# Performance work log

Hardware: AMD Instinct MI355X
Metric: run time of the kernel (lower is better)

## Reference

```python
import jax, jax.numpy as jnp
import numpy as np

DIM = 2048
N_HEADS = 16
HEAD_DIM = 128
EPS = 1e-6


def setup_inputs() -> dict:
    key = jax.random.key(0)
    ks = jax.random.split(key, 8)
    b, gf, gh, gw = 1, 8, 16, 24
    s = gf * gh * gw
    c = HEAD_DIM // 2
    w = lambda k: 0.02 * jax.random.normal(k, (DIM, DIM), jnp.float32)
    return {
        "x": jax.random.normal(ks[0], (b, s, DIM), jnp.float32),
        "freqs_angle": jax.random.normal(ks[1], (1024, c), jnp.float32),
        "Wq": w(ks[2]), "bq": jnp.zeros((DIM,), jnp.float32),
        "Wk": w(ks[3]), "bk": jnp.zeros((DIM,), jnp.float32),
        "Wv": w(ks[4]), "bv": jnp.zeros((DIM,), jnp.float32),
        "Wo": w(ks[5]), "bo": jnp.zeros((DIM,), jnp.float32),
        "gq": jnp.ones((DIM,), jnp.float32),
        "gk": jnp.ones((DIM,), jnp.float32),
        "seq_len": s, "grid_f": gf, "grid_h": gh, "grid_w": gw,
    }


def _rms(t, g):
    return t * jax.lax.rsqrt(jnp.mean(t * t, axis=-1, keepdims=True) + EPS) * g


def _grid_angles(freqs_angle, gf, gh, gw, c):
    # band split [c - 2*(c//3), c//3, c//3] as in rope_apply
    cf = c - 2 * (c // 3)
    ch = cw = c // 3
    af = freqs_angle[:gf, :cf]            # [F, cf]
    ah = freqs_angle[:gh, cf:cf + ch]     # [H, ch]
    aw = freqs_angle[:gw, cf + ch:c]      # [W, cw]
    ang = jnp.concatenate([
        jnp.broadcast_to(af[:, None, None, :], (gf, gh, gw, cf)),
        jnp.broadcast_to(ah[None, :, None, :], (gf, gh, gw, ch)),
        jnp.broadcast_to(aw[None, None, :, :], (gf, gh, gw, cw)),
    ], axis=-1)
    return ang.reshape(gf * gh * gw, c)   # [s, c]


def reference(x, freqs_angle, Wq, bq, Wk, bk, Wv, bv, Wo, bo, gq, gk,
              seq_len, grid_f, grid_h, grid_w):
    b, s, _ = x.shape
    n, d = N_HEADS, HEAD_DIM
    c = d // 2
    ang = _grid_angles(freqs_angle, grid_f, grid_h, grid_w, c)
    cos = jnp.cos(ang)[None, :, None, :]  # [1, s, 1, c]
    sin = jnp.sin(ang)[None, :, None, :]

    def rope(t):  # complex multiply on (even, odd) = (real, imag) pairs
        te, to = t[..., 0::2], t[..., 1::2]
        return jnp.stack([te * cos - to * sin, te * sin + to * cos], axis=-1).reshape(t.shape)

    q = _rms(x @ Wq.T + bq, gq).reshape(b, s, n, d)
    k = _rms(x @ Wk.T + bk, gk).reshape(b, s, n, d)
    v = (x @ Wv.T + bv).reshape(b, s, n, d)
    q, k = rope(q), rope(k)

    scale = np.float32(1.0 / np.sqrt(d))
    scores = jnp.einsum('bqnd,bknd->bnqk', q, k) * scale
    p = jax.nn.softmax(scores, axis=-1)
    o = jnp.einsum('bnqk,bknd->bqnd', p, v).reshape(b, s, n * d)
    return o @ Wo.T + bo
```

## Files before the change

kernel.cpp:

```cpp
#include <hip/hip_runtime.h>
#include <stdint.h>
#include <stddef.h>

typedef __bf16 bf16_t;
typedef __bf16 bf16x8 __attribute__((ext_vector_type(8)));
typedef __bf16 bf16x4 __attribute__((ext_vector_type(4)));
typedef __bf16 bf16x2 __attribute__((ext_vector_type(2)));
typedef float  f32x4  __attribute__((ext_vector_type(4)));

#define SEQ   3072
#define DIMD  2048
#define NH    16
#define HD    128
#define QKVN  6144

__device__ __forceinline__ void async16(const bf16_t* g, bf16_t* l) {
  __builtin_amdgcn_global_load_lds((const __attribute__((address_space(1))) uint32_t*)g,
                                   (__attribute__((address_space(3))) uint32_t*)l, 16, 0, 0);
}

__global__ __launch_bounds__(256) void cvt_all(const float* __restrict__ x,
                                               const float* __restrict__ Wq,
                                               const float* __restrict__ Wk,
                                               const float* __restrict__ Wv,
                                               const float* __restrict__ Wo,
                                               const float* __restrict__ bq,
                                               const float* __restrict__ bk,
                                               const float* __restrict__ bv,
                                               bf16_t* __restrict__ xb,
                                               bf16_t* __restrict__ Wqkvb,
                                               bf16_t* __restrict__ Wob,
                                               float* __restrict__ bqkv) {
  const int b = blockIdx.x;
  const float* src; bf16_t* dst; int off;
  if (b < 3072)       { src = x;  dst = xb;              off = b; }
  else if (b < 5120)  { src = Wq; dst = Wqkvb;           off = b - 3072; }
  else if (b < 7168)  { src = Wk; dst = Wqkvb + 4194304; off = b - 5120; }
  else if (b < 9216)  { src = Wv; dst = Wqkvb + 8388608; off = b - 7168; }
  else if (b < 11264) { src = Wo; dst = Wob;             off = b - 9216; }
  else {
    int t = (b - 11264) * 256 + threadIdx.x;
    float v;
    if (t < 2048)      v = bq[t];
    else if (t < 4096) v = bk[t - 2048];
    else               v = bv[t - 4096];
    bqkv[t] = v;
    return;
  }
  const int idx = (off * 256 + threadIdx.x) * 8;
  const float4 a = *(const float4*)(src + idx);
  const float4 c = *(const float4*)(src + idx + 4);
  bf16x8 o;
  o[0] = (bf16_t)a.x; o[1] = (bf16_t)a.y; o[2] = (bf16_t)a.z; o[3] = (bf16_t)a.w;
  o[4] = (bf16_t)c.x; o[5] = (bf16_t)c.y; o[6] = (bf16_t)c.z; o[7] = (bf16_t)c.w;
  *(bf16x8*)(dst + idx) = o;
}

template<bool OUT_BF16>
__global__ __launch_bounds__(256, 2) void gemm_nt(const bf16_t* __restrict__ A,
                                                  const bf16_t* __restrict__ B,
                                                  const float* __restrict__ bias,
                                                  void* __restrict__ Cout,
                                                  int M, int N, int K) {
  __shared__ __align__(16) bf16_t As[128 * 64];
  __shared__ __align__(16) bf16_t Bs[128 * 64];
  const int t = threadIdx.x;
  const int lane = t & 63, wave = t >> 6;
  const int quad = lane >> 4, l15 = lane & 15;
  const int wy = wave >> 1, wx = wave & 1;
  const size_t bm = (size_t)blockIdx.y * 128, bn = (size_t)blockIdx.x * 128;
  const bf16_t* Ab = A + bm * K;
  const bf16_t* Bb = B + bn * K;
  f32x4 acc[4][4] = {};
  int srow[4], scol[4];
#pragma unroll
  for (int r = 0; r < 4; r++) {
    int L = r * 256 + t;
    int row = L >> 3, cp = L & 7;
    srow[r] = row;
    scol[r] = (cp ^ (row & 7)) * 8;
  }
  for (int k0 = 0; k0 < K; k0 += 64) {
    __syncthreads();
#pragma unroll
    for (int r = 0; r < 4; r++)
      async16(Ab + (size_t)srow[r] * K + k0 + scol[r], &As[(r * 256 + t) * 8]);
#pragma unroll
    for (int r = 0; r < 4; r++)
      async16(Bb + (size_t)srow[r] * K + k0 + scol[r], &Bs[(r * 256 + t) * 8]);
    __syncthreads();
#pragma unroll
    for (int ks = 0; ks < 2; ks++) {
      bf16x8 af[4], bfv[4];
#pragma unroll
      for (int i = 0; i < 4; i++) {
        int row = wy * 64 + i * 16 + l15;
        af[i] = *(const bf16x8*)&As[row * 64 + (((ks * 4 + quad) ^ (row & 7)) * 8)];
      }
#pragma unroll
      for (int j = 0; j < 4; j++) {
        int row = wx * 64 + j * 16 + l15;
        bfv[j] = *(const bf16x8*)&Bs[row * 64 + (((ks * 4 + quad) ^ (row & 7)) * 8)];
      }
#pragma unroll
      for (int i = 0; i < 4; i++)
#pragma unroll
        for (int j = 0; j < 4; j++)
          acc[i][j] = __builtin_amdgcn_mfma_f32_16x16x32_bf16(af[i], bfv[j], acc[i][j], 0, 0, 0);
    }
  }
#pragma unroll
  for (int i = 0; i < 4; i++) {
#pragma unroll
    for (int j = 0; j < 4; j++) {
      size_t row = bm + wy * 64 + i * 16 + quad * 4;
      size_t col = bn + wx * 64 + j * 16 + l15;
      float bb = bias[col];
#pragma unroll
      for (int r = 0; r < 4; r++) {
        float v = acc[i][j][r] + bb;
        if (OUT_BF16) ((bf16_t*)Cout)[(row + r) * N + col] = (bf16_t)v;
        else          ((float*)Cout)[(row + r) * N + col] = v;
      }
    }
  }
}

__global__ __launch_bounds__(256) void rmsrope(bf16_t* __restrict__ qkv,
                                               bf16_t* __restrict__ pk,
                                               const float* __restrict__ gq,
                                               const float* __restrict__ gk,
                                               const float* __restrict__ freqs) {
  const int s = blockIdx.x, t = threadIdx.x;
  bf16_t* row = qkv + (size_t)s * QKVN;
  bf16x8 qv = *(const bf16x8*)&row[t * 8];
  bf16x8 kv = *(const bf16x8*)&row[2048 + t * 8];
  float qf[8], kf[8];
  float qs = 0.f, ks2 = 0.f;
#pragma unroll
  for (int i = 0; i < 8; i++) {
    qf[i] = (float)qv[i]; qs  += qf[i] * qf[i];
    kf[i] = (float)kv[i]; ks2 += kf[i] * kf[i];
  }
#pragma unroll
  for (int m = 1; m < 64; m <<= 1) {
    qs  += __shfl_xor(qs, m);
    ks2 += __shfl_xor(ks2, m);
  }
  __shared__ float red[2][4];
  const int wave = t >> 6, lane = t & 63;
  if (lane == 0) { red[0][wave] = qs; red[1][wave] = ks2; }
  __syncthreads();
  qs  = red[0][0] + red[0][1] + red[0][2] + red[0][3];
  ks2 = red[1][0] + red[1][1] + red[1][2] + red[1][3];
  const float qsc = rsqrtf(qs  / 2048.f + 1e-6f);
  const float ksc = rsqrtf(ks2 / 2048.f + 1e-6f);
  const int sf = s / 384, rem = s - sf * 384;
  const int sh = rem / 24, sw = rem - sh * 24;
  bf16x8 qo, ko;
#pragma unroll
  for (int u = 0; u < 4; u++) {
    const int col = t * 8 + 2 * u;
    const int i = (col >> 1) & 63;
    const int frow = (i < 22) ? sf : ((i < 43) ? sh : sw);
    const float ang = freqs[frow * 64 + i];
    float sn, cs;
    __sincosf(ang, &sn, &cs);
    float te = qf[2 * u]     * qsc * gq[col];
    float to = qf[2 * u + 1] * qsc * gq[col + 1];
    qo[2 * u]     = (bf16_t)(te * cs - to * sn);
    qo[2 * u + 1] = (bf16_t)(te * sn + to * cs);
    te = kf[2 * u]     * ksc * gk[col];
    to = kf[2 * u + 1] * ksc * gk[col + 1];
    ko[2 * u]     = (bf16_t)(te * cs - to * sn);
    ko[2 * u + 1] = (bf16_t)(te * sn + to * cs);
  }
  *(bf16x8*)&row[t * 8] = qo;
  *(bf16x8*)&pk[((size_t)(t >> 4) * SEQ + s) * HD + (t & 15) * 8] = ko;
}

__global__ __launch_bounds__(256) void vtrans(const bf16_t* __restrict__ qkv,
                                              bf16_t* __restrict__ pvt) {
  __shared__ bf16_t tile[128][65];
  const int h = blockIdx.y;
  const int s0 = blockIdx.x * 64;
  const int t = threadIdx.x;
#pragma unroll
  for (int r = 0; r < 4; r++) {
    int L = r * 256 + t, s = L >> 4, cp = L & 15;
    bf16x8 v = *(const bf16x8*)&qkv[(size_t)(s0 + s) * QKVN + 4096 + h * HD + cp * 8];
#pragma unroll
    for (int i = 0; i < 8; i++) tile[cp * 8 + i][s] = v[i];
  }
  __syncthreads();
#pragma unroll
  for (int r = 0; r < 4; r++) {
    int L = r * 256 + t, d = L >> 3, c = L & 7;
    bf16x8 o;
#pragma unroll
    for (int i = 0; i < 8; i++) o[i] = tile[d][c * 8 + i];
    *(bf16x8*)&pvt[((size_t)h * HD + d) * SEQ + s0 + c * 8] = o;
  }
}

__global__ __launch_bounds__(256, 2) void flash_attn(const bf16_t* __restrict__ qkv,
                                                     const bf16_t* __restrict__ pk,
                                                     const bf16_t* __restrict__ pvt,
                                                     bf16_t* __restrict__ ob) {
  __shared__ __align__(16) bf16_t Ks[2][64 * 128];
  __shared__ __align__(16) bf16_t Vt[2][128 * 64];
  __shared__ __align__(16) bf16_t Ps[4][32 * 64];
  const int h = blockIdx.y, qt = blockIdx.x;
  const int s0 = qt * 128;
  const int t = threadIdx.x, wave = t >> 6, lane = t & 63;
  const int quad = lane >> 4, l15 = lane & 15;
  const int wq = wave * 32;
  const float scale = 0.08838834764831845f;
  const bf16_t* pkh = pk  + (size_t)h * (SEQ * HD);
  const bf16_t* pvh = pvt + (size_t)h * (HD * SEQ);
  int krow4[4], kc4[4], vd4[4], vc4[4];
#pragma unroll
  for (int r = 0; r < 4; r++) {
    int L = r * 256 + t;
    krow4[r] = L >> 4; kc4[r] = (L & 15) ^ (krow4[r] & 7);
    vd4[r]   = L >> 3; vc4[r] = (L & 7)  ^ (vd4[r] & 7);
  }
  bf16x8 qfr[2][4];
#pragma unroll
  for (int tj = 0; tj < 2; tj++)
#pragma unroll
    for (int ks = 0; ks < 4; ks++)
      qfr[tj][ks] = *(const bf16x8*)&qkv[(size_t)(s0 + wq + tj * 16 + l15) * QKVN + h * HD + ks * 32 + quad * 8];
  f32x4 oacc[2][8] = {};
  float m_run[2] = {-3e38f, -3e38f}, l_run[2] = {0.f, 0.f};
#pragma unroll
  for (int r = 0; r < 4; r++) {
    int L = r * 256 + t;
    async16(pkh + (size_t)krow4[r] * HD + kc4[r] * 8, &Ks[0][L * 8]);
  }
#pragma unroll
  for (int r = 0; r < 4; r++) {
    int L = r * 256 + t;
    async16(pvh + (size_t)vd4[r] * SEQ + vc4[r] * 8, &Vt[0][L * 8]);
  }
  for (int kt = 0; kt < SEQ / 64; kt++) {
    const int cur = kt & 1;
    __syncthreads();
    if (kt + 1 < SEQ / 64) {
      const int kv1 = (kt + 1) * 64;
#pragma unroll
      for (int r = 0; r < 4; r++) {
        int L = r * 256 + t;
        async16(pkh + (size_t)(kv1 + krow4[r]) * HD + kc4[r] * 8, &Ks[cur ^ 1][L * 8]);
      }
#pragma unroll
      for (int r = 0; r < 4; r++) {
        int L = r * 256 + t;
        async16(pvh + (size_t)vd4[r] * SEQ + kv1 + vc4[r] * 8, &Vt[cur ^ 1][L * 8]);
      }
    }
    f32x4 st[4][2] = {};
#pragma unroll
    for (int ks = 0; ks < 4; ks++) {
      bf16x8 kfr[4];
#pragma unroll
      for (int ti = 0; ti < 4; ti++) {
        const int kr = ti * 16 + l15;
        kfr[ti] = *(const bf16x8*)&Ks[cur][kr * 128 + (((ks * 4 + quad) ^ (kr & 7)) * 8)];
      }
#pragma unroll
      for (int ti = 0; ti < 4; ti++)
#pragma unroll
        for (int tj = 0; tj < 2; tj++)
          st[ti][tj] = __builtin_amdgcn_mfma_f32_16x16x32_bf16(kfr[ti], qfr[tj][ks], st[ti][tj], 0, 0, 0);
    }
    float mt[2] = {-3e38f, -3e38f};
#pragma unroll
    for (int ti = 0; ti < 4; ti++)
#pragma unroll
      for (int tj = 0; tj < 2; tj++)
#pragma unroll
        for (int r = 0; r < 4; r++) {
          st[ti][tj][r] *= scale;
          mt[tj] = fmaxf(mt[tj], st[ti][tj][r]);
        }
    float al[2];
#pragma unroll
    for (int tj = 0; tj < 2; tj++) {
      mt[tj] = fmaxf(mt[tj], __shfl_xor(mt[tj], 16));
      mt[tj] = fmaxf(mt[tj], __shfl_xor(mt[tj], 32));
      const float mn = fmaxf(m_run[tj], mt[tj]);
      al[tj] = __expf(m_run[tj] - mn);
      m_run[tj] = mn;
    }
    float lt[2] = {0.f, 0.f};
#pragma unroll
    for (int ti = 0; ti < 4; ti++)
#pragma unroll
      for (int tj = 0; tj < 2; tj++) {
        bf16x4 pv;
#pragma unroll
        for (int r = 0; r < 4; r++) {
          const float p = __expf(st[ti][tj][r] - m_run[tj]);
          pv[r] = (bf16_t)p;
          lt[tj] += (float)pv[r];
        }
        const int q = tj * 16 + l15;
        const int cp2 = (ti * 2 + (quad >> 1)) ^ (q & 7);
        *(bf16x4*)&Ps[wave][q * 64 + cp2 * 8 + (quad & 1) * 4] = pv;
      }
#pragma unroll
    for (int tj = 0; tj < 2; tj++) {
      lt[tj] += __shfl_xor(lt[tj], 16);
      lt[tj] += __shfl_xor(lt[tj], 32);
      l_run[tj] = l_run[tj] * al[tj] + lt[tj];
    }
#pragma unroll
    for (int ti = 0; ti < 2; ti++) {
      float a0 = __shfl(al[ti], quad * 4 + 0);
      float a1 = __shfl(al[ti], quad * 4 + 1);
      float a2 = __shfl(al[ti], quad * 4 + 2);
      float a3 = __shfl(al[ti], quad * 4 + 3);
#pragma unroll
      for (int dj = 0; dj < 8; dj++) {
        oacc[ti][dj][0] *= a0; oacc[ti][dj][1] *= a1;
        oacc[ti][dj][2] *= a2; oacc[ti][dj][3] *= a3;
      }
    }
#pragma unroll
    for (int ks = 0; ks < 2; ks++) {
      bf16x8 pf[2], vf[8];
#pragma unroll
      for (int ti = 0; ti < 2; ti++) {
        const int q = ti * 16 + l15;
        pf[ti] = *(const bf16x8*)&Ps[wave][q * 64 + (((ks * 4 + quad) ^ (q & 7)) * 8)];
      }
#pragma unroll
      for (int dj = 0; dj < 8; dj++) {
        const int d = dj * 16 + l15;
        vf[dj] = *(const bf16x8*)&Vt[cur][d * 64 + (((ks * 4 + quad) ^ (d & 7)) * 8)];
      }
#pragma unroll
      for (int ti = 0; ti < 2; ti++)
#pragma unroll
        for (int dj = 0; dj < 8; dj++)
          oacc[ti][dj] = __builtin_amdgcn_mfma_f32_16x16x32_bf16(pf[ti], vf[dj], oacc[ti][dj], 0, 0, 0);
    }
  }
#pragma unroll
  for (int ti = 0; ti < 2; ti++) {
    float li[4];
#pragma unroll
    for (int r = 0; r < 4; r++) li[r] = 1.f / __shfl(l_run[ti], quad * 4 + r);
#pragma unroll
    for (int dj = 0; dj < 8; dj++)
#pragma unroll
      for (int r = 0; r < 4; r++) {
        const float v = oacc[ti][dj][r] * li[r];
        ob[(size_t)(s0 + wq + ti * 16 + quad * 4 + r) * DIMD + h * HD + dj * 16 + l15] = (bf16_t)v;
      }
  }
}

extern "C" void kernel_launch(void* const* d_in, const int* in_sizes, int n_in,
                              void* d_out, int out_size, void* d_ws, size_t ws_size,
                              hipStream_t stream) {
  (void)in_sizes; (void)n_in; (void)out_size;
  const float* x     = (const float*)d_in[0];
  const float* freqs = (const float*)d_in[1];
  const float* Wq    = (const float*)d_in[2];
  const float* bq    = (const float*)d_in[3];
  const float* Wk    = (const float*)d_in[4];
  const float* bk    = (const float*)d_in[5];
  const float* Wv    = (const float*)d_in[6];
  const float* bv    = (const float*)d_in[7];
  const float* Wo    = (const float*)d_in[8];
  const float* bo    = (const float*)d_in[9];
  const float* gq    = (const float*)d_in[10];
  const float* gk    = (const float*)d_in[11];

  char* w = (char*)d_ws;
  bf16_t* xb    = (bf16_t*)(w);
  bf16_t* Wqkvb = (bf16_t*)(w + 12582912);
  bf16_t* Wob   = (bf16_t*)(w + 37748736);
  bf16_t* qkvb  = (bf16_t*)(w + 46137344);
  bf16_t* obuf  = (bf16_t*)(w + 83886080);
  float*  bqkv  = (float*) (w + 96468992);
  bf16_t* pk    = (bf16_t*)(w);
  bf16_t* pvt   = (bf16_t*)(w + 12582912);
  if (ws_size < (size_t)96493568) return;

  cvt_all<<<11288, 256, 0, stream>>>(x, Wq, Wk, Wv, Wo, bq, bk, bv, xb, Wqkvb, Wob, bqkv);

  gemm_nt<true><<<dim3(48, 24), 256, 0, stream>>>(xb, Wqkvb, bqkv, qkvb, SEQ, QKVN, DIMD);
  rmsrope<<<3072, 256, 0, stream>>>(qkvb, pk, gq, gk, freqs);
  vtrans<<<dim3(48, NH), 256, 0, stream>>>(qkvb, pvt);
  flash_attn<<<dim3(24, NH), 256, 0, stream>>>(qkvb, pk, pvt, obuf);
  gemm_nt<false><<<dim3(16, 24), 256, 0, stream>>>(obuf, Wob, bo, (float*)d_out, SEQ, DIMD, DIMD);
}
```

Baseline: 444.2 us.

## Fold softmax scale into Q, use exp2, lazy rescale, 3-wave attention blocks

The attention scale and log2(e) are folded into the Q normalisation inside rmsrope, so the attention kernel can drop the per-score multiply and use the native exp2. The online-softmax accumulator rescale is skipped whenever the new tile max stays within 11.5 (log2 units) of the running max, which avoids the shuffles and output multiplies on most tiles. Blocks are cut from 4 waves to 3, with 96 queries each, giving 512 blocks instead of 384 for better spread across CUs. In exchange, the K/V staging loop is less even, and unnormalised probabilities can grow to about 2^11.5 before they are cast to bf16.

```diff
diff --git a/kernel.cpp b/kernel.cpp
--- a/kernel.cpp
+++ b/kernel.cpp
@@ -153,7 +153,7 @@
   __syncthreads();
   qs  = red[0][0] + red[0][1] + red[0][2] + red[0][3];
   ks2 = red[1][0] + red[1][1] + red[1][2] + red[1][3];
-  const float qsc = rsqrtf(qs  / 2048.f + 1e-6f);
+  const float qsc = rsqrtf(qs  / 2048.f + 1e-6f) * 0.12751745f;
   const float ksc = rsqrtf(ks2 / 2048.f + 1e-6f);
   const int sf = s / 384, rem = s - sf * 384;
   const int sh = rem / 24, sw = rem - sh * 24;
@@ -203,27 +203,42 @@
   }
 }
 
-__global__ __launch_bounds__(256, 2) void flash_attn(const bf16_t* __restrict__ qkv,
+#define STAGE_KV(BUF, KV1) do {                                              \
+    _Pragma("unroll")                                                        \
+    for (int r = 0; r < 5; r++) {                                            \
+      int L = r * 192 + t;                                                   \
+      async16(pkh + (size_t)(KV1) * HD + koff[r], &Ks[BUF][L * 8]);          \
+      async16(pvh + (KV1) + voff[r], &Vt[BUF][L * 8]);                       \
+    }                                                                        \
+    if (t < 64) {                                                            \
+      int L = 5 * 192 + t;                                                   \
+      async16(pkh + (size_t)(KV1) * HD + koff[5], &Ks[BUF][L * 8]);          \
+      async16(pvh + (KV1) + voff[5], &Vt[BUF][L * 8]);                       \
+    }                                                                        \
+  } while (0)
+
+__global__ __launch_bounds__(192, 2) void flash_attn(const bf16_t* __restrict__ qkv,
                                                      const bf16_t* __restrict__ pk,
                                                      const bf16_t* __restrict__ pvt,
                                                      bf16_t* __restrict__ ob) {
   __shared__ __align__(16) bf16_t Ks[2][64 * 128];
   __shared__ __align__(16) bf16_t Vt[2][128 * 64];
-  __shared__ __align__(16) bf16_t Ps[4][32 * 64];
+  __shared__ __align__(16) bf16_t Ps[3][32 * 64];
   const int h = blockIdx.y, qt = blockIdx.x;
-  const int s0 = qt * 128;
+  const int s0 = qt * 96;
   const int t = threadIdx.x, wave = t >> 6, lane = t & 63;
   const int quad = lane >> 4, l15 = lane & 15;
   const int wq = wave * 32;
-  const float scale = 0.08838834764831845f;
   const bf16_t* pkh = pk  + (size_t)h * (SEQ * HD);
   const bf16_t* pvh = pvt + (size_t)h * (HD * SEQ);
-  int krow4[4], kc4[4], vd4[4], vc4[4];
-#pragma unroll
-  for (int r = 0; r < 4; r++) {
-    int L = r * 256 + t;
-    krow4[r] = L >> 4; kc4[r] = (L & 15) ^ (krow4[r] & 7);
-    vd4[r]   = L >> 3; vc4[r] = (L & 7)  ^ (vd4[r] & 7);
+  int koff[6], voff[6];
+#pragma unroll
+  for (int r = 0; r < 6; r++) {
+    int L = r * 192 + t;
+    int krow = L >> 4, kc = (L & 15) ^ (krow & 7);
+    koff[r] = krow * HD + kc * 8;
+    int vd = L >> 3, vc = (L & 7) ^ (vd & 7);
+    voff[r] = vd * SEQ + vc * 8;
   }
   bf16x8 qfr[2][4];
 #pragma unroll
@@ -233,32 +248,11 @@
       qfr[tj][ks] = *(const bf16x8*)&qkv[(size_t)(s0 + wq + tj * 16 + l15) * QKVN + h * HD + ks * 32 + quad * 8];
   f32x4 oacc[2][8] = {};
   float m_run[2] = {-3e38f, -3e38f}, l_run[2] = {0.f, 0.f};
-#pragma unroll
-  for (int r = 0; r < 4; r++) {
-    int L = r * 256 + t;
-    async16(pkh + (size_t)krow4[r] * HD + kc4[r] * 8, &Ks[0][L * 8]);
-  }
-#pragma unroll
-  for (int r = 0; r < 4; r++) {
-    int L = r * 256 + t;
-    async16(pvh + (size_t)vd4[r] * SEQ + vc4[r] * 8, &Vt[0][L * 8]);
-  }
+  STAGE_KV(0, 0);
   for (int kt = 0; kt < SEQ / 64; kt++) {
     const int cur = kt & 1;
     __syncthreads();
-    if (kt + 1 < SEQ / 64) {
-      const int kv1 = (kt + 1) * 64;
-#pragma unroll
-      for (int r = 0; r < 4; r++) {
-        int L = r * 256 + t;
-        async16(pkh + (size_t)(kv1 + krow4[r]) * HD + kc4[r] * 8, &Ks[cur ^ 1][L * 8]);
-      }
-#pragma unroll
-      for (int r = 0; r < 4; r++) {
-        int L = r * 256 + t;
-        async16(pvh + (size_t)vd4[r] * SEQ + kv1 + vc4[r] * 8, &Vt[cur ^ 1][L * 8]);
-      }
-    }
+    if (kt + 1 < SEQ / 64) STAGE_KV(cur ^ 1, (kt + 1) * 64);
     f32x4 st[4][2] = {};
 #pragma unroll
     for (int ks = 0; ks < 4; ks++) {
@@ -280,18 +274,21 @@
 #pragma unroll
       for (int tj = 0; tj < 2; tj++)
 #pragma unroll
-        for (int r = 0; r < 4; r++) {
-          st[ti][tj][r] *= scale;
+        for (int r = 0; r < 4; r++)
           mt[tj] = fmaxf(mt[tj], st[ti][tj][r]);
-        }
-    float al[2];
+    float al[2]; bool resc[2];
 #pragma unroll
     for (int tj = 0; tj < 2; tj++) {
       mt[tj] = fmaxf(mt[tj], __shfl_xor(mt[tj], 16));
       mt[tj] = fmaxf(mt[tj], __shfl_xor(mt[tj], 32));
-      const float mn = fmaxf(m_run[tj], mt[tj]);
-      al[tj] = __expf(m_run[tj] - mn);
-      m_run[tj] = mn;
+      if (__all(mt[tj] <= m_run[tj] + 11.5f)) {
+        al[tj] = 1.f; resc[tj] = false;
+      } else {
+        const float mn = fmaxf(m_run[tj], mt[tj]);
+        al[tj] = __builtin_amdgcn_exp2f(m_run[tj] - mn);
+        m_run[tj] = mn;
+        resc[tj] = true;
+      }
     }
     float lt[2] = {0.f, 0.f};
 #pragma unroll
@@ -301,7 +298,7 @@
         bf16x4 pv;
 #pragma unroll
         for (int r = 0; r < 4; r++) {
-          const float p = __expf(st[ti][tj][r] - m_run[tj]);
+          const float p = __builtin_amdgcn_exp2f(st[ti][tj][r] - m_run[tj]);
           pv[r] = (bf16_t)p;
           lt[tj] += (float)pv[r];
         }
@@ -317,14 +314,16 @@
     }
 #pragma unroll
     for (int ti = 0; ti < 2; ti++) {
-      float a0 = __shfl(al[ti], quad * 4 + 0);
-      float a1 = __shfl(al[ti], quad * 4 + 1);
-      float a2 = __shfl(al[ti], quad * 4 + 2);
-      float a3 = __shfl(al[ti], quad * 4 + 3);
-#pragma unroll
-      for (int dj = 0; dj < 8; dj++) {
-        oacc[ti][dj][0] *= a0; oacc[ti][dj][1] *= a1;
-        oacc[ti][dj][2] *= a2; oacc[ti][dj][3] *= a3;
+      if (resc[ti]) {
+        float a0 = __shfl(al[ti], quad * 4 + 0);
+        float a1 = __shfl(al[ti], quad * 4 + 1);
+        float a2 = __shfl(al[ti], quad * 4 + 2);
+        float a3 = __shfl(al[ti], quad * 4 + 3);
+#pragma unroll
+        for (int dj = 0; dj < 8; dj++) {
+          oacc[ti][dj][0] *= a0; oacc[ti][dj][1] *= a1;
+          oacc[ti][dj][2] *= a2; oacc[ti][dj][3] *= a3;
+        }
       }
     }
 #pragma unroll
@@ -395,6 +394,6 @@
   gemm_nt<true><<<dim3(48, 24), 256, 0, stream>>>(xb, Wqkvb, bqkv, qkvb, SEQ, QKVN, DIMD);
   rmsrope<<<3072, 256, 0, stream>>>(qkvb, pk, gq, gk, freqs);
   vtrans<<<dim3(48, NH), 256, 0, stream>>>(qkvb, pvt);
-  flash_attn<<<dim3(24, NH), 256, 0, stream>>>(qkvb, pk, pvt, obuf);
+  flash_attn<<<dim3(32, NH), 192, 0, stream>>>(qkvb, pk, pvt, obuf);
   gemm_nt<false><<<dim3(16, 24), 256, 0, stream>>>(obuf, Wob, bo, (float*)d_out, SEQ, DIMD, DIMD);
 }
```

Measured after the change: 432.8 us. 1.03x faster.
